# Kernel tuning notes

Measured on AMD Instinct MI355X. Metric: run time of the kernel, lower is better.

The kernel has to match this reference:

```python
import jax, jax.numpy as jnp
import numpy as np

D_MODEL = 1024
NHEAD = 16
D_K = D_MODEL // NHEAD
THETA_NC = 0.01
B, S = 2, 2048

def setup_inputs() -> dict:
    key = jax.random.key(0)
    ks = jax.random.split(key, 8)
    lim = 1.0 / np.sqrt(D_MODEL)
    return {
        "x": jax.random.normal(ks[0], (B, S, D_MODEL), dtype=jnp.float32),
        "Wq": jax.random.uniform(ks[1], (D_MODEL, D_MODEL), jnp.float32, -lim, lim),
        "Wk": jax.random.uniform(ks[2], (D_MODEL, D_MODEL), jnp.float32, -lim, lim),
        "Wv": jax.random.uniform(ks[3], (D_MODEL, D_MODEL), jnp.float32, -lim, lim),
        "Wo": jax.random.uniform(ks[4], (D_MODEL, D_MODEL), jnp.float32, -lim, lim),
        "bo": jnp.zeros((D_MODEL,), jnp.float32),
        "gauge_phase": jnp.zeros((NHEAD,), jnp.float32),
        "gauge_amplitude": jnp.ones((NHEAD,), jnp.float32),
        "nc_mixing": jax.random.normal(ks[5], (NHEAD, D_K, D_K), jnp.float32) * THETA_NC,
    }

def reference(x, Wq, Wk, Wv, Wo, bo, gauge_phase, gauge_amplitude, nc_mixing):
    b, s, _ = x.shape
    # QKV projections (torch Linear: x @ W.T), reshape to [b, h, s, d_k]
    def proj(W):
        return (x @ W.T).reshape(b, s, NHEAD, D_K).transpose(0, 2, 1, 3)
    Q, K, V = proj(Wq), proj(Wk), proj(Wv)
    # gauge: real part of exp(i*phase) is cos(phase); amplitude scale per head
    g = (gauge_amplitude * jnp.cos(gauge_phase)).reshape(1, NHEAD, 1, 1)
    Q_nc = jnp.einsum('bhnd,hdk->bhnk', Q * g, nc_mixing)
    K_nc = jnp.einsum('bhnd,hdk->bhnk', K * g, nc_mixing)
    scores = jnp.einsum('bhnk,bhmk->bhnm', Q_nc, K_nc) / jnp.sqrt(jnp.float32(D_K))
    attn = jax.nn.softmax(scores, axis=-1)
    ctx = jnp.einsum('bhnm,bhmd->bhnd', attn, V)
    ctx = ctx.transpose(0, 2, 1, 3).reshape(b, s, D_MODEL)
    out = ctx @ Wo.T + bo
    return out, attn
```

## Files before the change

### kernel.cpp

```cpp
#include <hip/hip_runtime.h>

typedef short bf16x8 __attribute__((ext_vector_type(8)));
typedef float f32x4 __attribute__((ext_vector_type(4)));
typedef unsigned short u16;

__device__ __forceinline__ u16 f2bf(float f) {
  union { float f; unsigned u; } v; v.f = f;
  unsigned r = v.u + 0x7fffu + ((v.u >> 16) & 1u);
  return (u16)(r >> 16);
}
__device__ __forceinline__ float bf2f(u16 s) {
  union { unsigned u; float f; } v; v.u = ((unsigned)s) << 16;
  return v.f;
}

__global__ __launch_bounds__(256) void fold_kernel(
    const float* __restrict__ Wq, const float* __restrict__ Wk,
    const float* __restrict__ phase, const float* __restrict__ amp,
    const float* __restrict__ nc,
    u16* __restrict__ WqE, u16* __restrict__ WkE) {
  __shared__ float ncS[64 * 64];
  __shared__ float WS[64 * 65];
  int bid = blockIdx.x;
  int sel = bid >> 8, h = (bid >> 4) & 15, d0 = (bid & 15) * 64;
  const float* W = sel ? Wk : Wq;
  u16* O = sel ? WkE : WqE;
  float g = amp[h] * cosf(phase[h]);
  float sc = g * (sel ? 1.0f : 0.125f * 1.44269504088896f);
  int t = threadIdx.x;
  for (int l = t; l < 4096; l += 256) ncS[l] = nc[h * 4096 + l];
  for (int l = t; l < 4096; l += 256) {
    int e = l >> 6, dd = l & 63;
    WS[e * 65 + dd] = W[(h * 64 + e) * 1024 + d0 + dd];
  }
  __syncthreads();
  int kp = t >> 2, q = t & 3;
  for (int dd = q * 16; dd < q * 16 + 16; ++dd) {
    float acc = 0.f;
#pragma unroll
    for (int e = 0; e < 64; ++e) acc += WS[e * 65 + dd] * ncS[e * 64 + kp];
    O[(h * 64 + kp) * 1024 + d0 + dd] = f2bf(acc * sc);
  }
}

__global__ __launch_bounds__(256) void cast_kernel(const float* __restrict__ src,
                                                   u16* __restrict__ dst, int n4) {
  int i = blockIdx.x * 256 + threadIdx.x;
  if (i >= n4) return;
  float4 v = ((const float4*)src)[i];
  ushort4 o;
  o.x = f2bf(v.x); o.y = f2bf(v.y); o.z = f2bf(v.z); o.w = f2bf(v.w);
  ((ushort4*)dst)[i] = o;
}

__global__ __launch_bounds__(256) void split_kernel(const float* __restrict__ src,
                                                    u16* __restrict__ hi, u16* __restrict__ lo, int n4) {
  int i = blockIdx.x * 256 + threadIdx.x;
  if (i >= n4) return;
  float4 v = ((const float4*)src)[i];
  ushort4 h, l;
  h.x = f2bf(v.x); l.x = f2bf(v.x - bf2f(h.x));
  h.y = f2bf(v.y); l.y = f2bf(v.y - bf2f(h.y));
  h.z = f2bf(v.z); l.z = f2bf(v.z - bf2f(h.z));
  h.w = f2bf(v.w); l.w = f2bf(v.w - bf2f(h.w));
  ((ushort4*)hi)[i] = h;
  ((ushort4*)lo)[i] = l;
}

#define LDA 72
__global__ __launch_bounds__(256) void proj_gemm(
    const u16* __restrict__ A, const u16* __restrict__ W0, const u16* __restrict__ W1,
    const u16* __restrict__ W2, u16* __restrict__ Qnc, u16* __restrict__ Knc,
    u16* __restrict__ Vt) {
  __shared__ u16 As[128 * LDA];
  __shared__ u16 Bs[128 * LDA];
  int z = blockIdx.z;
  const u16* Wp = (z == 0) ? W0 : ((z == 1) ? W1 : W2);
  int m0 = blockIdx.x * 128, n0 = blockIdx.y * 128;
  int t = threadIdx.x, lane = t & 63, wid = t >> 6;
  int wr = wid >> 1, wc = wid & 1;
  f32x4 acc[4][4] = {};
  bf16x8 pa[4], pb[4];
#pragma unroll
  for (int it = 0; it < 4; ++it) {
    int q = it * 256 + t;
    int row = q >> 3, c8 = (q & 7) * 8;
    pa[it] = *(const bf16x8*)&A[(m0 + row) * 1024 + c8];
    pb[it] = *(const bf16x8*)&Wp[(n0 + row) * 1024 + c8];
  }
  for (int k0 = 0; k0 < 1024; k0 += 64) {
    __syncthreads();
#pragma unroll
    for (int it = 0; it < 4; ++it) {
      int q = it * 256 + t;
      int row = q >> 3, c8 = (q & 7) * 8;
      *(bf16x8*)&As[row * LDA + c8] = pa[it];
      *(bf16x8*)&Bs[row * LDA + c8] = pb[it];
    }
    __syncthreads();
    if (k0 + 64 < 1024) {
#pragma unroll
      for (int it = 0; it < 4; ++it) {
        int q = it * 256 + t;
        int row = q >> 3, c8 = (q & 7) * 8;
        pa[it] = *(const bf16x8*)&A[(m0 + row) * 1024 + k0 + 64 + c8];
        pb[it] = *(const bf16x8*)&Wp[(n0 + row) * 1024 + k0 + 64 + c8];
      }
    }
#pragma unroll
    for (int kk = 0; kk < 2; ++kk) {
      bf16x8 af2[4], bfr2[4];
#pragma unroll
      for (int m = 0; m < 4; ++m) {
        af2[m] = *(const bf16x8*)&As[(wr * 64 + m * 16 + (lane & 15)) * LDA + kk * 32 + (lane >> 4) * 8];
        bfr2[m] = *(const bf16x8*)&Bs[(wc * 64 + m * 16 + (lane & 15)) * LDA + kk * 32 + (lane >> 4) * 8];
      }
#pragma unroll
      for (int m = 0; m < 4; ++m)
#pragma unroll
        for (int n = 0; n < 4; ++n)
          acc[m][n] = __builtin_amdgcn_mfma_f32_16x16x32_bf16(af2[m], bfr2[n], acc[m][n], 0, 0, 0);
    }
  }
#pragma unroll
  for (int m = 0; m < 4; ++m)
#pragma unroll
    for (int n = 0; n < 4; ++n)
#pragma unroll
      for (int rr = 0; rr < 4; ++rr) {
        int row = m0 + wr * 64 + m * 16 + (lane >> 4) * 4 + rr;
        int col = n0 + wc * 64 + n * 16 + (lane & 15);
        u16 v = f2bf(acc[m][n][rr]);
        int bh = (row >> 11) * 16 + (col >> 6);
        if (z == 2)
          Vt[bh * 131072 + (col & 63) * 2048 + (row & 2047)] = v;
        else if (z == 0)
          Qnc[bh * 131072 + (row & 2047) * 64 + (col & 63)] = v;
        else
          Knc[bh * 131072 + (row & 2047) * 64 + (col & 63)] = v;
      }
}

#define PSTRIDE 72
__global__ __launch_bounds__(512, 4) void attn_kernel(
    const u16* __restrict__ Qnc, const u16* __restrict__ Knc, const u16* __restrict__ Vt,
    u16* __restrict__ ctxh, float* __restrict__ attn_out) {
  __shared__ u16 Ks[4096];
  __shared__ u16 Vs[4096];
  __shared__ u16 P[8][16 * PSTRIDE];
  int t = threadIdx.x, lane = t & 63, wid = t >> 6;
  int g = lane >> 4, li = lane & 15;
  int ord = blockIdx.x;
  int lid = ((ord & 7) << 6) + (ord >> 3);
  int bh = lid >> 4;
  int i0 = (lid & 15) * 128 + wid * 16;
  const u16* Qp = Qnc + bh * 131072;
  const u16* Kp = Knc + bh * 131072;
  const u16* Vp = Vt + bh * 131072;
  u16* Pw = &P[wid][0];

  int srow = (wid << 3) + (lane >> 3);
  int scol8 = lane & 7;
  int sdst = srow * 64 + (((scol8 ^ (srow & 7)) << 3));

  bf16x8 qf0 = *(const bf16x8*)&Qp[(i0 + li) * 64 + g * 8];
  bf16x8 qf1 = *(const bf16x8*)&Qp[(i0 + li) * 64 + 32 + g * 8];

  float l[4] = {0.f, 0.f, 0.f, 0.f};
  {
    bf16x8 kreg = *(const bf16x8*)&Kp[srow * 64 + scol8 * 8];
    for (int s0 = 0; s0 < 2048; s0 += 64) {
      __syncthreads();
      *(bf16x8*)&Ks[sdst] = kreg;
      __syncthreads();
      if (s0 + 64 < 2048)
        kreg = *(const bf16x8*)&Kp[(s0 + 64 + srow) * 64 + scol8 * 8];
#pragma unroll
      for (int ct = 0; ct < 4; ++ct) {
        int jr = ct * 16 + li;
        bf16x8 kf0 = *(const bf16x8*)&Ks[jr * 64 + ((g ^ (jr & 7)) << 3)];
        bf16x8 kf1 = *(const bf16x8*)&Ks[jr * 64 + (((4 + g) ^ (jr & 7)) << 3)];
        f32x4 a = {};
        a = __builtin_amdgcn_mfma_f32_16x16x32_bf16(qf0, kf0, a, 0, 0, 0);
        a = __builtin_amdgcn_mfma_f32_16x16x32_bf16(qf1, kf1, a, 0, 0, 0);
#pragma unroll
        for (int rr = 0; rr < 4; ++rr) l[rr] += __builtin_amdgcn_exp2f(a[rr]);
      }
    }
  }
  float rinv[4];
#pragma unroll
  for (int rr = 0; rr < 4; ++rr) {
    float s = l[rr];
#pragma unroll
    for (int off = 1; off < 16; off <<= 1) s += __shfl_xor(s, off);
    rinv[rr] = 1.0f / s;
  }

  f32x4 ctx[4] = {};
  float* ao = attn_out + (size_t)bh * 4194304;
  int rrow = lane >> 4;
  int rcol = (lane & 15) * 4;
  bf16x8 k2 = *(const bf16x8*)&Kp[srow * 64 + scol8 * 8];
  bf16x8 v2 = *(const bf16x8*)&Vp[srow * 2048 + scol8 * 8];
  for (int s0 = 0; s0 < 2048; s0 += 64) {
    __syncthreads();
    *(bf16x8*)&Ks[sdst] = k2;
    *(bf16x8*)&Vs[sdst] = v2;
    __syncthreads();
    if (s0 + 64 < 2048) {
      k2 = *(const bf16x8*)&Kp[(s0 + 64 + srow) * 64 + scol8 * 8];
      v2 = *(const bf16x8*)&Vp[srow * 2048 + s0 + 64 + scol8 * 8];
    }
    f32x4 acc[4];
#pragma unroll
    for (int ct = 0; ct < 4; ++ct) {
      int jr = ct * 16 + li;
      bf16x8 kf0 = *(const bf16x8*)&Ks[jr * 64 + ((g ^ (jr & 7)) << 3)];
      bf16x8 kf1 = *(const bf16x8*)&Ks[jr * 64 + (((4 + g) ^ (jr & 7)) << 3)];
      f32x4 a = {};
      a = __builtin_amdgcn_mfma_f32_16x16x32_bf16(qf0, kf0, a, 0, 0, 0);
      a = __builtin_amdgcn_mfma_f32_16x16x32_bf16(qf1, kf1, a, 0, 0, 0);
      acc[ct] = a;
    }
#pragma unroll
    for (int ct = 0; ct < 4; ++ct)
#pragma unroll
      for (int rr = 0; rr < 4; ++rr) {
        float p = __builtin_amdgcn_exp2f(acc[ct][rr]) * rinv[rr];
        Pw[(g * 4 + rr) * PSTRIDE + ct * 16 + li] = f2bf(p);
      }
    bf16x8 pa0 = *(const bf16x8*)&Pw[li * PSTRIDE + g * 8];
    bf16x8 pa1 = *(const bf16x8*)&Pw[li * PSTRIDE + 32 + g * 8];
#pragma unroll
    for (int j = 0; j < 4; ++j) {
      int row = j * 4 + rrow;
      ushort4 pv4 = *(const ushort4*)&Pw[row * PSTRIDE + rcol];
      f32x4 o = {bf2f(pv4.x), bf2f(pv4.y), bf2f(pv4.z), bf2f(pv4.w)};
      __builtin_nontemporal_store(o, (f32x4*)&ao[(size_t)(i0 + row) * 2048 + s0 + rcol]);
    }
#pragma unroll
    for (int dt = 0; dt < 4; ++dt) {
      int d = dt * 16 + li;
      bf16x8 vf0 = *(const bf16x8*)&Vs[d * 64 + ((g ^ (d & 7)) << 3)];
      bf16x8 vf1 = *(const bf16x8*)&Vs[d * 64 + (((4 + g) ^ (d & 7)) << 3)];
      ctx[dt] = __builtin_amdgcn_mfma_f32_16x16x32_bf16(pa0, vf0, ctx[dt], 0, 0, 0);
      ctx[dt] = __builtin_amdgcn_mfma_f32_16x16x32_bf16(pa1, vf1, ctx[dt], 0, 0, 0);
    }
  }
  int b = bh >> 4, hh = bh & 15;
#pragma unroll
  for (int dt = 0; dt < 4; ++dt)
#pragma unroll
    for (int rr = 0; rr < 4; ++rr) {
      int q = i0 + g * 4 + rr;
      int idx = (b * 2048 + q) * 1024 + hh * 64 + dt * 16 + li;
      ctxh[idx] = f2bf(ctx[dt][rr]);
    }
}

#define LDO 72
__global__ __launch_bounds__(256) void outproj_gemm(
    const u16* __restrict__ ch, const u16* __restrict__ wh, const u16* __restrict__ wl,
    const float* __restrict__ bo, float* __restrict__ out) {
  __shared__ u16 Ah[128 * LDO], Bh[64 * LDO], Bl[64 * LDO];
  int m0 = blockIdx.x * 128, n0 = blockIdx.y * 64;
  int t = threadIdx.x, lane = t & 63, wid = t >> 6;
  int wr = wid >> 1, wc = wid & 1;
  f32x4 acc[4][2] = {};
  bf16x8 pa[4], pbh[2], pbl[2];
#pragma unroll
  for (int it = 0; it < 4; ++it) {
    int q = it * 256 + t;
    int row = q >> 3, c8 = (q & 7) * 8;
    pa[it] = *(const bf16x8*)&ch[(m0 + row) * 1024 + c8];
  }
#pragma unroll
  for (int it = 0; it < 2; ++it) {
    int q = it * 256 + t;
    int row = q >> 3, c8 = (q & 7) * 8;
    pbh[it] = *(const bf16x8*)&wh[(n0 + row) * 1024 + c8];
    pbl[it] = *(const bf16x8*)&wl[(n0 + row) * 1024 + c8];
  }
  for (int k0 = 0; k0 < 1024; k0 += 64) {
    __syncthreads();
#pragma unroll
    for (int it = 0; it < 4; ++it) {
      int q = it * 256 + t;
      int row = q >> 3, c8 = (q & 7) * 8;
      *(bf16x8*)&Ah[row * LDO + c8] = pa[it];
    }
#pragma unroll
    for (int it = 0; it < 2; ++it) {
      int q = it * 256 + t;
      int row = q >> 3, c8 = (q & 7) * 8;
      *(bf16x8*)&Bh[row * LDO + c8] = pbh[it];
      *(bf16x8*)&Bl[row * LDO + c8] = pbl[it];
    }
    __syncthreads();
    if (k0 + 64 < 1024) {
#pragma unroll
      for (int it = 0; it < 4; ++it) {
        int q = it * 256 + t;
        int row = q >> 3, c8 = (q & 7) * 8;
        pa[it] = *(const bf16x8*)&ch[(m0 + row) * 1024 + k0 + 64 + c8];
      }
#pragma unroll
      for (int it = 0; it < 2; ++it) {
        int q = it * 256 + t;
        int row = q >> 3, c8 = (q & 7) * 8;
        pbh[it] = *(const bf16x8*)&wh[(n0 + row) * 1024 + k0 + 64 + c8];
        pbl[it] = *(const bf16x8*)&wl[(n0 + row) * 1024 + k0 + 64 + c8];
      }
    }
#pragma unroll
    for (int kk = 0; kk < 2; ++kk) {
      bf16x8 ah[4], bhf[2], blf[2];
#pragma unroll
      for (int m = 0; m < 4; ++m)
        ah[m] = *(const bf16x8*)&Ah[(wr * 64 + m * 16 + (lane & 15)) * LDO + kk * 32 + (lane >> 4) * 8];
#pragma unroll
      for (int n = 0; n < 2; ++n) {
        int br = (wc * 32 + n * 16 + (lane & 15)) * LDO + kk * 32 + (lane >> 4) * 8;
        bhf[n] = *(const bf16x8*)&Bh[br];
        blf[n] = *(const bf16x8*)&Bl[br];
      }
#pragma unroll
      for (int m = 0; m < 4; ++m)
#pragma unroll
        for (int n = 0; n < 2; ++n) {
          acc[m][n] = __builtin_amdgcn_mfma_f32_16x16x32_bf16(ah[m], bhf[n], acc[m][n], 0, 0, 0);
          acc[m][n] = __builtin_amdgcn_mfma_f32_16x16x32_bf16(ah[m], blf[n], acc[m][n], 0, 0, 0);
        }
    }
  }
#pragma unroll
  for (int m = 0; m < 4; ++m)
#pragma unroll
    for (int n = 0; n < 2; ++n)
#pragma unroll
      for (int rr = 0; rr < 4; ++rr) {
        int row = m0 + wr * 64 + m * 16 + (lane >> 4) * 4 + rr;
        int col = n0 + wc * 32 + n * 16 + (lane & 15);
        out[row * 1024 + col] = acc[m][n][rr] + bo[col];
      }
}

extern "C" void kernel_launch(void* const* d_in, const int* in_sizes, int n_in,
                              void* d_out, int out_size, void* d_ws, size_t ws_size,
                              hipStream_t stream) {
  const float* x = (const float*)d_in[0];
  const float* Wq = (const float*)d_in[1];
  const float* Wk = (const float*)d_in[2];
  const float* Wv = (const float*)d_in[3];
  const float* Wo = (const float*)d_in[4];
  const float* bo = (const float*)d_in[5];
  const float* phase = (const float*)d_in[6];
  const float* amp = (const float*)d_in[7];
  const float* nc = (const float*)d_in[8];

  float* out0 = (float*)d_out;
  float* attn = out0 + 4194304;

  u16* x_bf = (u16*)d_ws;
  u16* Qnc = x_bf + 4194304;
  u16* Knc = Qnc + 4194304;
  u16* Vt = Knc + 4194304;
  u16* ctxh = Vt + 4194304;
  u16* WqE = ctxh + 4194304;
  u16* WkE = WqE + 1048576;
  u16* Wvb = WkE + 1048576;
  u16* Woh = Wvb + 1048576;
  u16* Wol = Woh + 1048576;

  fold_kernel<<<dim3(512), dim3(256), 0, stream>>>(Wq, Wk, phase, amp, nc, WqE, WkE);
  cast_kernel<<<dim3(4096), dim3(256), 0, stream>>>(x, x_bf, 1048576);
  cast_kernel<<<dim3(1024), dim3(256), 0, stream>>>(Wv, Wvb, 262144);
  split_kernel<<<dim3(1024), dim3(256), 0, stream>>>(Wo, Woh, Wol, 262144);
  proj_gemm<<<dim3(32, 8, 3), dim3(256), 0, stream>>>(x_bf, WqE, WkE, Wvb, Qnc, Knc, Vt);
  attn_kernel<<<dim3(512), dim3(512), 0, stream>>>(Qnc, Knc, Vt, ctxh, attn);
  outproj_gemm<<<dim3(32, 16), dim3(256), 0, stream>>>(ctxh, Woh, Wol, bo, out0);
}
```

Baseline: 234.5 us.

## Use direct global-to-LDS loads with swizzle in projection GEMM; drop Wo hi/lo split

The projection GEMM now loads tiles directly from global memory into LDS via global_load_lds with an XOR-swizzled layout, replacing register staging and the padded layout. The register-level prefetch of the next tile is removed, so load latency is no longer overlapped with MFMA work inside a block. The output projection uses a single bf16 cast of Wo instead of a hi/lo split. This halves that GEMM's MFMAs and weight traffic at the cost of reduced precision.

```diff
diff --git a/kernel.cpp b/kernel.cpp
--- a/kernel.cpp
+++ b/kernel.cpp
@@ -12,6 +12,10 @@
 __device__ __forceinline__ float bf2f(u16 s) {
   union { unsigned u; float f; } v; v.u = ((unsigned)s) << 16;
   return v.f;
+}
+__device__ __forceinline__ void gload16(const void* g, void* l) {
+  __builtin_amdgcn_global_load_lds((const __attribute__((address_space(1))) void*)g,
+                                   (__attribute__((address_space(3))) void*)l, 16, 0, 0);
 }
 
 __global__ __launch_bounds__(256) void fold_kernel(
@@ -53,67 +57,40 @@
   ((ushort4*)dst)[i] = o;
 }
 
-__global__ __launch_bounds__(256) void split_kernel(const float* __restrict__ src,
-                                                    u16* __restrict__ hi, u16* __restrict__ lo, int n4) {
-  int i = blockIdx.x * 256 + threadIdx.x;
-  if (i >= n4) return;
-  float4 v = ((const float4*)src)[i];
-  ushort4 h, l;
-  h.x = f2bf(v.x); l.x = f2bf(v.x - bf2f(h.x));
-  h.y = f2bf(v.y); l.y = f2bf(v.y - bf2f(h.y));
-  h.z = f2bf(v.z); l.z = f2bf(v.z - bf2f(h.z));
-  h.w = f2bf(v.w); l.w = f2bf(v.w - bf2f(h.w));
-  ((ushort4*)hi)[i] = h;
-  ((ushort4*)lo)[i] = l;
-}
-
-#define LDA 72
 __global__ __launch_bounds__(256) void proj_gemm(
     const u16* __restrict__ A, const u16* __restrict__ W0, const u16* __restrict__ W1,
     const u16* __restrict__ W2, u16* __restrict__ Qnc, u16* __restrict__ Knc,
     u16* __restrict__ Vt) {
-  __shared__ u16 As[128 * LDA];
-  __shared__ u16 Bs[128 * LDA];
+  __shared__ u16 As[128 * 64];
+  __shared__ u16 Bs[128 * 64];
   int z = blockIdx.z;
   const u16* Wp = (z == 0) ? W0 : ((z == 1) ? W1 : W2);
   int m0 = blockIdx.x * 128, n0 = blockIdx.y * 128;
-  int t = threadIdx.x, lane = t & 63, wid = t >> 6;
+  int t = threadIdx.x, lane = t & 63;
+  int wid = t >> 6;
   int wr = wid >> 1, wc = wid & 1;
+  int li = lane & 15, g = lane >> 4;
   f32x4 acc[4][4] = {};
-  bf16x8 pa[4], pb[4];
-#pragma unroll
-  for (int it = 0; it < 4; ++it) {
-    int q = it * 256 + t;
-    int row = q >> 3, c8 = (q & 7) * 8;
-    pa[it] = *(const bf16x8*)&A[(m0 + row) * 1024 + c8];
-    pb[it] = *(const bf16x8*)&Wp[(n0 + row) * 1024 + c8];
-  }
   for (int k0 = 0; k0 < 1024; k0 += 64) {
     __syncthreads();
 #pragma unroll
     for (int it = 0; it < 4; ++it) {
-      int q = it * 256 + t;
-      int row = q >> 3, c8 = (q & 7) * 8;
-      *(bf16x8*)&As[row * LDA + c8] = pa[it];
-      *(bf16x8*)&Bs[row * LDA + c8] = pb[it];
-    }
-    __syncthreads();
-    if (k0 + 64 < 1024) {
-#pragma unroll
-      for (int it = 0; it < 4; ++it) {
-        int q = it * 256 + t;
-        int row = q >> 3, c8 = (q & 7) * 8;
-        pa[it] = *(const bf16x8*)&A[(m0 + row) * 1024 + k0 + 64 + c8];
-        pb[it] = *(const bf16x8*)&Wp[(n0 + row) * 1024 + k0 + 64 + c8];
-      }
-    }
+      int u = it * 256 + t;
+      int row = u >> 3, c8 = u & 7;
+      int scu = (c8 ^ (row & 7)) * 8;
+      gload16(&A[(m0 + row) * 1024 + k0 + scu], &As[u * 8]);
+      gload16(&Wp[(n0 + row) * 1024 + k0 + scu], &Bs[u * 8]);
+    }
+    __syncthreads();
 #pragma unroll
     for (int kk = 0; kk < 2; ++kk) {
       bf16x8 af2[4], bfr2[4];
 #pragma unroll
       for (int m = 0; m < 4; ++m) {
-        af2[m] = *(const bf16x8*)&As[(wr * 64 + m * 16 + (lane & 15)) * LDA + kk * 32 + (lane >> 4) * 8];
-        bfr2[m] = *(const bf16x8*)&Bs[(wc * 64 + m * 16 + (lane & 15)) * LDA + kk * 32 + (lane >> 4) * 8];
+        int ra = wr * 64 + m * 16 + li;
+        int rb = wc * 64 + m * 16 + li;
+        af2[m] = *(const bf16x8*)&As[ra * 64 + (((kk * 4 + g) ^ (ra & 7)) << 3)];
+        bfr2[m] = *(const bf16x8*)&Bs[rb * 64 + (((kk * 4 + g) ^ (rb & 7)) << 3)];
       }
 #pragma unroll
       for (int m = 0; m < 4; ++m)
@@ -261,14 +238,14 @@
 
 #define LDO 72
 __global__ __launch_bounds__(256) void outproj_gemm(
-    const u16* __restrict__ ch, const u16* __restrict__ wh, const u16* __restrict__ wl,
+    const u16* __restrict__ ch, const u16* __restrict__ wh,
     const float* __restrict__ bo, float* __restrict__ out) {
-  __shared__ u16 Ah[128 * LDO], Bh[64 * LDO], Bl[64 * LDO];
+  __shared__ u16 Ah[128 * LDO], Bh[64 * LDO];
   int m0 = blockIdx.x * 128, n0 = blockIdx.y * 64;
   int t = threadIdx.x, lane = t & 63, wid = t >> 6;
   int wr = wid >> 1, wc = wid & 1;
   f32x4 acc[4][2] = {};
-  bf16x8 pa[4], pbh[2], pbl[2];
+  bf16x8 pa[4], pbh[2];
 #pragma unroll
   for (int it = 0; it < 4; ++it) {
     int q = it * 256 + t;
@@ -280,7 +257,6 @@
     int q = it * 256 + t;
     int row = q >> 3, c8 = (q & 7) * 8;
     pbh[it] = *(const bf16x8*)&wh[(n0 + row) * 1024 + c8];
-    pbl[it] = *(const bf16x8*)&wl[(n0 + row) * 1024 + c8];
   }
   for (int k0 = 0; k0 < 1024; k0 += 64) {
     __syncthreads();
@@ -295,7 +271,6 @@
       int q = it * 256 + t;
       int row = q >> 3, c8 = (q & 7) * 8;
       *(bf16x8*)&Bh[row * LDO + c8] = pbh[it];
-      *(bf16x8*)&Bl[row * LDO + c8] = pbl[it];
     }
     __syncthreads();
     if (k0 + 64 < 1024) {
@@ -310,28 +285,22 @@
         int q = it * 256 + t;
         int row = q >> 3, c8 = (q & 7) * 8;
         pbh[it] = *(const bf16x8*)&wh[(n0 + row) * 1024 + k0 + 64 + c8];
-        pbl[it] = *(const bf16x8*)&wl[(n0 + row) * 1024 + k0 + 64 + c8];
       }
     }
 #pragma unroll
     for (int kk = 0; kk < 2; ++kk) {
-      bf16x8 ah[4], bhf[2], blf[2];
+      bf16x8 ah[4], bhf[2];
 #pragma unroll
       for (int m = 0; m < 4; ++m)
         ah[m] = *(const bf16x8*)&Ah[(wr * 64 + m * 16 + (lane & 15)) * LDO + kk * 32 + (lane >> 4) * 8];
 #pragma unroll
-      for (int n = 0; n < 2; ++n) {
-        int br = (wc * 32 + n * 16 + (lane & 15)) * LDO + kk * 32 + (lane >> 4) * 8;
-        bhf[n] = *(const bf16x8*)&Bh[br];
-        blf[n] = *(const bf16x8*)&Bl[br];
-      }
+      for (int n = 0; n < 2; ++n)
+        bhf[n] = *(const bf16x8*)&Bh[(wc * 32 + n * 16 + (lane & 15)) * LDO + kk * 32 + (lane >> 4) * 8];
 #pragma unroll
       for (int m = 0; m < 4; ++m)
 #pragma unroll
-        for (int n = 0; n < 2; ++n) {
+        for (int n = 0; n < 2; ++n)
           acc[m][n] = __builtin_amdgcn_mfma_f32_16x16x32_bf16(ah[m], bhf[n], acc[m][n], 0, 0, 0);
-          acc[m][n] = __builtin_amdgcn_mfma_f32_16x16x32_bf16(ah[m], blf[n], acc[m][n], 0, 0, 0);
-        }
     }
   }
 #pragma unroll
@@ -370,14 +339,13 @@
   u16* WqE = ctxh + 4194304;
   u16* WkE = WqE + 1048576;
   u16* Wvb = WkE + 1048576;
-  u16* Woh = Wvb + 1048576;
-  u16* Wol = Woh + 1048576;
+  u16* Wob = Wvb + 1048576;
 
   fold_kernel<<<dim3(512), dim3(256), 0, stream>>>(Wq, Wk, phase, amp, nc, WqE, WkE);
   cast_kernel<<<dim3(4096), dim3(256), 0, stream>>>(x, x_bf, 1048576);
   cast_kernel<<<dim3(1024), dim3(256), 0, stream>>>(Wv, Wvb, 262144);
-  split_kernel<<<dim3(1024), dim3(256), 0, stream>>>(Wo, Woh, Wol, 262144);
+  cast_kernel<<<dim3(1024), dim3(256), 0, stream>>>(Wo, Wob, 262144);
   proj_gemm<<<dim3(32, 8, 3), dim3(256), 0, stream>>>(x_bf, WqE, WkE, Wvb, Qnc, Knc, Vt);
   attn_kernel<<<dim3(512), dim3(512), 0, stream>>>(Qnc, Knc, Vt, ctxh, attn);
-  outproj_gemm<<<dim3(32, 16), dim3(256), 0, stream>>>(ctxh, Woh, Wol, bo, out0);
-}
+  outproj_gemm<<<dim3(32, 16), dim3(256), 0, stream>>>(ctxh, Wob, bo, out0);
+}
```

Result: no change. 234.6 us (+0.0%).
